# Optimization experiments

Hardware: AMD Instinct MI355X
Metric: run time of the kernel (lower is better)

## Reference

```python
import jax, jax.numpy as jnp
import numpy as np

K = 3          # kernel_size
STRIDE = 1
BLOCK = 64     # block_size
OUT_FEATURES = 512
IN_CH = 256
IN_FEATURES = K * K * IN_CH          # 2304
Q = IN_FEATURES // BLOCK             # 36 (exact)
P = OUT_FEATURES // BLOCK            # 8


def _unfold(x, k, stride):
    # torch F.unfold with padding=k//2: output (B, C*k*k, Ho*Wo),
    # feature order channel-major then (di, dj)
    B, C, H, W = x.shape
    pad = k // 2
    xp = jnp.pad(x, ((0, 0), (0, 0), (pad, pad), (pad, pad)))
    Ho = (H + 2 * pad - k) // stride + 1
    Wo = (W + 2 * pad - k) // stride + 1
    cols = jnp.stack(
        [xp[:, :, di:di + (Ho - 1) * stride + 1:stride,
                  dj:dj + (Wo - 1) * stride + 1:stride]
         for di in range(k) for dj in range(k)],
        axis=2)  # (B, C, k*k, Ho, Wo)
    return cols.reshape(B, C * k * k, Ho * Wo), Ho, Wo


def setup_inputs() -> dict:
    key = jax.random.key(0)
    k1, k2 = jax.random.split(key)
    x = jax.random.normal(k1, (8, IN_CH, 32, 32), dtype=jnp.float32)
    # xavier-uniform-like init on (p, q, block)
    fan_in, fan_out = Q * BLOCK, P * BLOCK
    a = float(np.sqrt(6.0 / (fan_in + fan_out)))
    weight = jax.random.uniform(k2, (P, Q, BLOCK), dtype=jnp.float32,
                                minval=-a, maxval=a)
    return {"x": x, "weight": weight}


def reference(x, weight):
    B = x.shape[0]
    H = x.shape[2]
    xu, Ho, Wo = _unfold(x, K, STRIDE)          # (B, in_features, L)
    pad_rows = Q * BLOCK - IN_FEATURES          # 0 here, kept for faithfulness
    xu = jnp.pad(xu, ((0, 0), (0, pad_rows), (0, 0)))
    # faithful to torch reshape semantics (row-major over (B, q*b, L))
    xb = xu.reshape(-1, Q, BLOCK)               # (N, q, b), N = B*L
    xf = jnp.fft.rfft(xb)                       # (N, q, bf)
    wf = jnp.fft.rfft(weight)                   # (p, q, bf)
    hf = jnp.sum(xf[:, None, :, :] * wf[None, :, :, :], axis=2)  # (N, p, bf)
    h = jnp.fft.irfft(hf, n=BLOCK)              # (N, p, b)
    h = h.reshape(-1, P * BLOCK)
    if P * BLOCK > OUT_FEATURES:
        h = h[:, :OUT_FEATURES]
    L = (H // STRIDE) * (H // STRIDE)
    h = h.reshape(B, L, OUT_FEATURES)
    h = jnp.transpose(h, (0, 2, 1))
    return h.reshape(B, OUT_FEATURES, H // STRIDE, H // STRIDE)
```

## Files before the change

### kernel.cpp

```cpp
#include <hip/hip_runtime.h>
#include <hip/hip_bf16.h>


#define QK 2304
#define MROWS 8192
#define NOC 512
#define QB 36

typedef __attribute__((ext_vector_type(8))) short short8;
typedef __attribute__((ext_vector_type(4))) float floatx4;

__device__ __forceinline__ ushort f2bf(float f) {
    __hip_bfloat16 h = __float2bfloat16(f);
    return *reinterpret_cast<ushort*>(&h);
}

__device__ __forceinline__ void async16(const void* g, void* l) {
    __builtin_amdgcn_global_load_lds((const __attribute__((address_space(1))) void*)g,
                                     (__attribute__((address_space(3))) void*)l, 16, 0, 0);
}

#define PREP_A_BLOCKS 2048
#define PREP_B_BLOCKS 576

__global__ __launch_bounds__(256) void bcc_prep(const float* __restrict__ x,
                                                const float* __restrict__ w,
                                                ushort* __restrict__ wsA,
                                                ushort* __restrict__ wsB) {
    if (blockIdx.x < PREP_A_BLOCKS) {
        __shared__ float img[1024];
        const int bb = blockIdx.x >> 8, c = blockIdx.x & 255;
        const float* src = x + ((size_t)bb * 256 + c) * 1024;
        *(float4*)&img[threadIdx.x * 4] = *(const float4*)&src[threadIdx.x * 4];
        __syncthreads();

        const int loc0 = threadIdx.x * 4;
        ushort* dstbase = wsA + ((size_t)bb * 2304 + c * 9) * 1024 + loc0;
        #pragma unroll
        for (int kk = 0; kk < 9; ++kk) {
            const int di = kk / 3, dj = kk - di * 3;
            const int off = (di - 1) * 32 + (dj - 1);
            const bool row_ok = (unsigned)((loc0 >> 5) + di - 1) < 32u;
            ushort u[4];
            #pragma unroll
            for (int e = 0; e < 4; ++e) {
                int wi = ((loc0 + e) & 31) + dj - 1;
                bool ok = row_ok && ((unsigned)wi < 32u);
                float v = ok ? img[loc0 + e + off] : 0.f;
                u[e] = f2bf(v);
            }
            *(ushort4*)&dstbase[(size_t)kk * 1024] = make_ushort4(u[0], u[1], u[2], u[3]);
        }
    } else {
        int t = (blockIdx.x - PREP_A_BLOCKS) * 256 + threadIdx.x;
        int n = t / 288;
        int o = t - n * 288;
        int p = n >> 6, tt = n & 63;
        int k0 = o * 8;
        ushort u[8];
        #pragma unroll
        for (int e = 0; e < 8; ++e) {
            int k = k0 + e;
            int q = k >> 6, s = k & 63;
            u[e] = f2bf(w[(p * QB + q) * 64 + ((tt - s) & 63)]);
        }
        *(ushort4*)&wsB[(size_t)n * QK + k0]     = make_ushort4(u[0], u[1], u[2], u[3]);
        *(ushort4*)&wsB[(size_t)n * QK + k0 + 4] = make_ushort4(u[4], u[5], u[6], u[7]);
    }
}

__global__ __launch_bounds__(512) void bcc_mfma(const ushort* __restrict__ A,
                                                const ushort* __restrict__ Bm,
                                                float* __restrict__ out) {
    __shared__ ushort smem[3][2][128 * 64];

    const int tid = threadIdx.x;
    const int l = tid & 63, w = tid >> 6;
    const int t3 = w & 3, ks = w >> 2;
    const int wm = t3 & 1, wn = t3 >> 1;

    const int lin = blockIdx.x;
    const int n_idx = (lin >> 3) & 3;
    const int m_idx = ((lin >> 5) << 3) | (lin & 7);
    const int n0 = n_idx * 128;
    const int m0 = m_idx * 128;
    const int b  = m0 >> 10, r0 = m0 & 1023;

    const int lr = l & 15, lq = l >> 4;
    const int lrow = l >> 3;
    const int lkoff = ((l & 7) ^ (lrow & 7)) * 8;

    floatx4 acc[4][4];
    #pragma unroll
    for (int i = 0; i < 4; ++i)
        #pragma unroll
        for (int j = 0; j < 4; ++j) acc[i][j] = (floatx4){0.f, 0.f, 0.f, 0.f};

    auto stage = [&](int q, int buf) {
        const int kb = q * 64;
        #pragma unroll
        for (int t = 0; t < 2; ++t) {
            int row8 = w * 16 + t * 8;
            async16(A  + ((size_t)(m0 + row8 + lrow) * QK + kb + lkoff),
                    &smem[buf][0][row8 * 64]);
            async16(Bm + ((size_t)(n0 + row8 + lrow) * QK + kb + lkoff),
                    &smem[buf][1][row8 * 64]);
        }
    };

    stage(0, 0);
    stage(1, 1);
    const int ca = ks * 4 + lq;
    for (int q = 0; q < QB; ++q) {
        const int buf = q % 3;
        if (q + 2 < QB) {
            stage(q + 2, (q + 2) % 3);
            asm volatile("s_waitcnt vmcnt(8)" ::: "memory");
        } else if (q + 1 < QB) {
            asm volatile("s_waitcnt vmcnt(4)" ::: "memory");
        } else {
            asm volatile("s_waitcnt vmcnt(0)" ::: "memory");
        }
        __builtin_amdgcn_s_barrier();
        asm volatile("" ::: "memory");

        short8 av[4], bv[4];
        #pragma unroll
        for (int i = 0; i < 4; ++i) {
            int Ra = wm * 64 + i * 16 + lr;
            av[i] = *(const short8*)&smem[buf][0][Ra * 64 + ((ca ^ (Ra & 7)) * 8)];
        }
        #pragma unroll
        for (int j = 0; j < 4; ++j) {
            int Rb = wn * 64 + j * 16 + lr;
            bv[j] = *(const short8*)&smem[buf][1][Rb * 64 + ((ca ^ (Rb & 7)) * 8)];
        }
        #pragma unroll
        for (int i = 0; i < 4; ++i)
            #pragma unroll
            for (int j = 0; j < 4; ++j)
                acc[i][j] = __builtin_amdgcn_mfma_f32_16x16x32_bf16(bv[j], av[i], acc[i][j], 0, 0, 0);

        asm volatile("" ::: "memory");
        __builtin_amdgcn_s_barrier();
    }

    __syncthreads();
    float* fsm = (float*)&smem[0][0][0];
    if (ks == 1) {
        #pragma unroll
        for (int i = 0; i < 4; ++i)
            #pragma unroll
            for (int j = 0; j < 4; ++j)
                *(floatx4*)&fsm[t3 * 4096 + (i * 4 + j) * 256 + l * 4] = acc[i][j];
    }
    __syncthreads();
    if (ks == 0) {
        #pragma unroll
        for (int i = 0; i < 4; ++i) {
            int rr = r0 + wm * 64 + i * 16 + lr;
            #pragma unroll
            for (int j = 0; j < 4; ++j) {
                floatx4 o4 = *(const floatx4*)&fsm[t3 * 4096 + (i * 4 + j) * 256 + l * 4];
                #pragma unroll
                for (int e = 0; e < 4; ++e) {
                    int oc = n0 + wn * 64 + j * 16 + lq * 4 + e;
                    out[((size_t)b * NOC + oc) * 1024 + rr] = acc[i][j][e] + o4[e];
                }
            }
        }
    }
}

__global__ __launch_bounds__(256) void bcc_gemm_f32(
    const float* __restrict__ x, const float* __restrict__ w,
    float* __restrict__ out) {
    __shared__ float Asf[64][68];
    __shared__ float Wsf[64][68];
    const int tid = threadIdx.x;
    const int tn = tid & 15, tm = tid >> 4;
    const int p = blockIdx.x;
    const int m0 = blockIdx.y * 64;
    const int b = m0 >> 10, r0 = m0 & 1023;
    const float* xb = x + (size_t)b * (256 * 32 * 32);
    float acc[4][4] = {};
    for (int q = 0; q < QB; ++q) {
        #pragma unroll
        for (int i = 0; i < 16; ++i) {
            int idx = i * 256 + tid;
            int s = idx & 63, mm = idx >> 6;
            int flat = (r0 + mm) * QK + q * 64 + s;
            int feat = flat >> 10, loc = flat & 1023;
            int c = feat / 9, kk = feat - c * 9;
            int hi = (loc >> 5) + (kk / 3) - 1;
            int wi = (loc & 31) + (kk % 3) - 1;
            float v = 0.0f;
            if ((unsigned)hi < 32u && (unsigned)wi < 32u)
                v = xb[(c * 32 + hi) * 32 + wi];
            Asf[mm][s] = v;
        }
        const float* wb = w + (p * QB + q) * 64;
        #pragma unroll
        for (int i = 0; i < 16; ++i) {
            int idx = i * 256 + tid;
            int t = idx & 63, s = idx >> 6;
            Wsf[s][t] = wb[(t - s) & 63];
        }
        __syncthreads();
        #pragma unroll
        for (int s0 = 0; s0 < 64; s0 += 4) {
            float4 a4[4], b4[4];
            #pragma unroll
            for (int i2 = 0; i2 < 4; ++i2)
                a4[i2] = *(const float4*)&Asf[tm * 4 + i2][s0];
            #pragma unroll
            for (int ss = 0; ss < 4; ++ss)
                b4[ss] = *(const float4*)&Wsf[s0 + ss][tn * 4];
            #pragma unroll
            for (int i2 = 0; i2 < 4; ++i2) {
                const float* av = (const float*)&a4[i2];
                #pragma unroll
                for (int ss = 0; ss < 4; ++ss) {
                    float a = av[ss];
                    acc[i2][0] += a * b4[ss].x;
                    acc[i2][1] += a * b4[ss].y;
                    acc[i2][2] += a * b4[ss].z;
                    acc[i2][3] += a * b4[ss].w;
                }
            }
        }
        __syncthreads();
    }
    float* outb = out + (size_t)b * NOC * 1024;
    const int r_base = r0 + tm * 4;
    #pragma unroll
    for (int j = 0; j < 4; ++j) {
        int oc = p * 64 + tn * 4 + j;
        float4 v = make_float4(acc[0][j], acc[1][j], acc[2][j], acc[3][j]);
        *(float4*)&outb[(size_t)oc * 1024 + r_base] = v;
    }
}

extern "C" void kernel_launch(void* const* d_in, const int* in_sizes, int n_in,
                              void* d_out, int out_size, void* d_ws, size_t ws_size,
                              hipStream_t stream) {
    const float* x = (const float*)d_in[0];
    const float* w = (const float*)d_in[1];
    float* out = (float*)d_out;

    const size_t bytesA = (size_t)MROWS * QK * sizeof(ushort);
    const size_t bytesB = (size_t)NOC * QK * sizeof(ushort);

    if (ws_size >= bytesA + bytesB) {
        ushort* wsA = (ushort*)d_ws;
        ushort* wsB = (ushort*)((char*)d_ws + bytesA);
        bcc_prep<<<PREP_A_BLOCKS + PREP_B_BLOCKS, 256, 0, stream>>>(x, w, wsA, wsB);
        bcc_mfma<<<256, 512, 0, stream>>>(wsA, wsB, out);
    } else {
        bcc_gemm_f32<<<dim3(8, MROWS / 64), 256, 0, stream>>>(x, w, out);
    }
}
```

Baseline: 94.02 us.

## Replace full im2col buffer with three column-shifted padded planes and implicit gather

The prep kernel no longer materialises the full 9x-expanded im2col matrix. It writes three column-shifted, row-padded bf16 copies of each input channel plane (one per dj), and the GEMM computes source addresses on the fly from the row/k index, with di handled as a row offset. This cuts the prep kernel's global writes and the workspace footprint roughly threefold. The cost is extra integer address arithmetic in the staging loop, and it relies on each 16-byte async load staying contiguous within one shifted plane row.

```diff
diff --git a/kernel.cpp b/kernel.cpp
--- a/kernel.cpp
+++ b/kernel.cpp
@@ -3,9 +3,10 @@
 
 
 #define QK 2304
-#define MROWS 8192
 #define NOC 512
 #define QB 36
+#define XPLN 1088
+#define MROWS_FALLBACK 8192
 
 typedef __attribute__((ext_vector_type(8))) short short8;
 typedef __attribute__((ext_vector_type(4))) float floatx4;
@@ -25,7 +26,7 @@
 
 __global__ __launch_bounds__(256) void bcc_prep(const float* __restrict__ x,
                                                 const float* __restrict__ w,
-                                                ushort* __restrict__ wsA,
+                                                ushort* __restrict__ wsX,
                                                 ushort* __restrict__ wsB) {
     if (blockIdx.x < PREP_A_BLOCKS) {
         __shared__ float img[1024];
@@ -34,22 +35,21 @@
         *(float4*)&img[threadIdx.x * 4] = *(const float4*)&src[threadIdx.x * 4];
         __syncthreads();
 
-        const int loc0 = threadIdx.x * 4;
-        ushort* dstbase = wsA + ((size_t)bb * 2304 + c * 9) * 1024 + loc0;
-        #pragma unroll
-        for (int kk = 0; kk < 9; ++kk) {
-            const int di = kk / 3, dj = kk - di * 3;
-            const int off = (di - 1) * 32 + (dj - 1);
-            const bool row_ok = (unsigned)((loc0 >> 5) + di - 1) < 32u;
+        for (int t = threadIdx.x; t < 816; t += 256) {
+            const int cp = t / 272;
+            const int rem = t - cp * 272;
+            const int i = rem >> 3, j0 = (rem & 7) * 4;
+            const int srow = i - 1;
+            const bool rok = (unsigned)srow < 32u;
             ushort u[4];
             #pragma unroll
             for (int e = 0; e < 4; ++e) {
-                int wi = ((loc0 + e) & 31) + dj - 1;
-                bool ok = row_ok && ((unsigned)wi < 32u);
-                float v = ok ? img[loc0 + e + off] : 0.f;
+                int scol = j0 + e + cp - 1;
+                float v = (rok && (unsigned)scol < 32u) ? img[srow * 32 + scol] : 0.f;
                 u[e] = f2bf(v);
             }
-            *(ushort4*)&dstbase[(size_t)kk * 1024] = make_ushort4(u[0], u[1], u[2], u[3]);
+            *(ushort4*)&wsX[((size_t)(cp * 2048 + bb * 256 + c)) * XPLN + i * 32 + j0] =
+                make_ushort4(u[0], u[1], u[2], u[3]);
         }
     } else {
         int t = (blockIdx.x - PREP_A_BLOCKS) * 256 + threadIdx.x;
@@ -69,7 +69,7 @@
     }
 }
 
-__global__ __launch_bounds__(512) void bcc_mfma(const ushort* __restrict__ A,
+__global__ __launch_bounds__(512) void bcc_mfma(const ushort* __restrict__ X,
                                                 const ushort* __restrict__ Bm,
                                                 float* __restrict__ out) {
     __shared__ ushort smem[3][2][128 * 64];
@@ -85,6 +85,7 @@
     const int n0 = n_idx * 128;
     const int m0 = m_idx * 128;
     const int b  = m0 >> 10, r0 = m0 & 1023;
+    const int bc0 = b << 8;
 
     const int lr = l & 15, lq = l >> 4;
     const int lrow = l >> 3;
@@ -98,12 +99,22 @@
 
     auto stage = [&](int q, int buf) {
         const int kb = q * 64;
+        const int r  = r0 + w * 16 + lrow;
+        const int fb = r * QK + kb + lkoff;
+        const int kf = fb >> 10, loc = fb & 1023;
+        const int c  = (kf * 7282) >> 16;
+        const int kk = kf - c * 9;
+        const int di = (kk * 11) >> 5;
+        const int dj = kk - di * 3;
+        const size_t ei = (size_t)((dj << 11) + bc0 + c) * XPLN
+                        + ((loc >> 5) + di) * 32 + (loc & 31);
+        const size_t bofs = (size_t)(n0 + w * 16 + lrow) * QK + kb + lkoff;
         #pragma unroll
         for (int t = 0; t < 2; ++t) {
-            int row8 = w * 16 + t * 8;
-            async16(A  + ((size_t)(m0 + row8 + lrow) * QK + kb + lkoff),
+            const int row8 = w * 16 + t * 8;
+            async16(X  + ei + t * 2176,
                     &smem[buf][0][row8 * 64]);
-            async16(Bm + ((size_t)(n0 + row8 + lrow) * QK + kb + lkoff),
+            async16(Bm + bofs + (size_t)t * 8 * QK,
                     &smem[buf][1][row8 * 64]);
         }
     };
@@ -248,15 +259,15 @@
     const float* w = (const float*)d_in[1];
     float* out = (float*)d_out;
 
-    const size_t bytesA = (size_t)MROWS * QK * sizeof(ushort);
+    const size_t bytesX = (size_t)3 * 2048 * XPLN * sizeof(ushort);
     const size_t bytesB = (size_t)NOC * QK * sizeof(ushort);
 
-    if (ws_size >= bytesA + bytesB) {
-        ushort* wsA = (ushort*)d_ws;
-        ushort* wsB = (ushort*)((char*)d_ws + bytesA);
-        bcc_prep<<<PREP_A_BLOCKS + PREP_B_BLOCKS, 256, 0, stream>>>(x, w, wsA, wsB);
-        bcc_mfma<<<256, 512, 0, stream>>>(wsA, wsB, out);
+    if (ws_size >= bytesX + bytesB) {
+        ushort* wsX = (ushort*)d_ws;
+        ushort* wsB = (ushort*)((char*)d_ws + bytesX);
+        bcc_prep<<<PREP_A_BLOCKS + PREP_B_BLOCKS, 256, 0, stream>>>(x, w, wsX, wsB);
+        bcc_mfma<<<256, 512, 0, stream>>>(wsX, wsB, out);
     } else {
-        bcc_gemm_f32<<<dim3(8, MROWS / 64), 256, 0, stream>>>(x, w, out);
-    }
-}
+        bcc_gemm_f32<<<dim3(8, MROWS_FALLBACK / 64), 256, 0, stream>>>(x, w, out);
+    }
+}
```

After: 93.87 us. No clear change (-0.2%).
